# Optimization experiments

Measured on AMD Instinct MI355X. Metric: run time of the kernel, lower is better.

Reference implementation:

```python
import jax, jax.numpy as jnp
import numpy as np
from jax import lax

T, B = 256, 64
VOCAB, D_EMBED, D_HIDDEN = 32000, 512, 1024


def setup_inputs() -> dict:
    key = jax.random.key(0)
    k1, k2, k3, k4 = jax.random.split(key, 4)
    x_seq = jax.random.randint(k1, (T, B), 0, VOCAB, dtype=jnp.int64) if jax.config.jax_enable_x64 else jax.random.randint(k1, (T, B), 0, VOCAB, dtype=jnp.int32)
    scale_e = 1.0
    scale_ih = 1.0 / np.sqrt(D_HIDDEN)
    return {
        "x_seq": x_seq,
        "embedding": jax.random.normal(k2, (VOCAB, D_EMBED), dtype=jnp.float32) * scale_e,
        "W_ih": jax.random.normal(k3, (4 * D_HIDDEN, D_EMBED), dtype=jnp.float32) * scale_ih,
        "W_hh": jax.random.normal(k4, (4 * D_HIDDEN, D_HIDDEN), dtype=jnp.float32) * scale_ih,
        "b_ih": jnp.zeros((4 * D_HIDDEN,), dtype=jnp.float32),
        "b_hh": jnp.zeros((4 * D_HIDDEN,), dtype=jnp.float32),
    }


def reference(x_seq, embedding, W_ih, W_hh, b_ih, b_hh):
    # e_seq: [T, B, E]
    e_seq = embedding[x_seq]
    B_ = x_seq.shape[1]
    H = W_hh.shape[1]
    # Precompute input projections for all timesteps in one big GEMM: [T, B, 4H]
    x_gates = jnp.einsum("tbe,ge->tbg", e_seq, W_ih) + b_ih + b_hh

    def step(carry, xg):
        h, c = carry
        gates = xg + h @ W_hh.T  # [B, 4H]
        i, f, g, o = jnp.split(gates, 4, axis=-1)  # PyTorch gate order i,f,g,o
        i = jax.nn.sigmoid(i)
        f = jax.nn.sigmoid(f)
        g = jnp.tanh(g)
        o = jax.nn.sigmoid(o)
        c_new = f * c + i * g
        h_new = o * jnp.tanh(c_new)
        return (h_new, c_new), h_new

    h0 = jnp.zeros((B_, H), dtype=e_seq.dtype)
    c0 = jnp.zeros((B_, H), dtype=e_seq.dtype)
    (h, c), outs = lax.scan(step, (h0, c0), x_gates)
    return outs, h, c
```

## Files before the change

### kernel.cpp

```cpp
#include <hip/hip_runtime.h>
#include <hip/hip_bf16.h>
#include <cstdint>
#include <cstddef>

#define T_STEPS 256
#define BATCH   64
#define DE      512
#define DH      1024
#define G4      4096
#define NBLK    128

typedef short  bf16x8 __attribute__((ext_vector_type(8)));
typedef float  f32x4  __attribute__((ext_vector_type(4)));
typedef unsigned long long u64;

__device__ __forceinline__ unsigned short bf_bits(__hip_bfloat16 h) {
    union { __hip_bfloat16 h; unsigned short u; } x; x.h = h; return x.u;
}
__device__ __forceinline__ float b2f(unsigned short u) {
    union { float f; unsigned v; } x; x.v = ((unsigned)u) << 16; return x.f;
}

__device__ __forceinline__ void async_copy16(const void* gsrc, void* ldst) {
    __builtin_amdgcn_global_load_lds(
        (const __attribute__((address_space(1))) unsigned int*)gsrc,
        (__attribute__((address_space(3))) unsigned int*)ldst,
        16, 0, 0);
}

__device__ __forceinline__ u64 llc_load64(const u64* p) {
    return __hip_atomic_load(p, __ATOMIC_RELAXED, __HIP_MEMORY_SCOPE_AGENT);
}
__device__ __forceinline__ void llc_store64(u64* p, u64 v) {
    __hip_atomic_store(p, v, __ATOMIC_RELAXED, __HIP_MEMORY_SCOPE_AGENT);
}
__device__ __forceinline__ unsigned llc_load32(const unsigned* p) {
    return __hip_atomic_load(p, __ATOMIC_RELAXED, __HIP_MEMORY_SCOPE_AGENT);
}
__device__ __forceinline__ void llc_store32(unsigned* p, unsigned v) {
    __hip_atomic_store(p, v, __ATOMIC_RELAXED, __HIP_MEMORY_SCOPE_AGENT);
}

__global__ void k_f32_to_bf16(const float* __restrict__ src,
                              __hip_bfloat16* __restrict__ dst, int n8) {
    int i = blockIdx.x * blockDim.x + threadIdx.x;
    if (i >= n8) return;
    const float4* s = (const float4*)src + (size_t)i * 2;
    float4 a = s[0], b = s[1];
    union { unsigned short u[8]; uint4 v; } o;
    o.u[0] = bf_bits(__float2bfloat16(a.x));
    o.u[1] = bf_bits(__float2bfloat16(a.y));
    o.u[2] = bf_bits(__float2bfloat16(a.z));
    o.u[3] = bf_bits(__float2bfloat16(a.w));
    o.u[4] = bf_bits(__float2bfloat16(b.x));
    o.u[5] = bf_bits(__float2bfloat16(b.y));
    o.u[6] = bf_bits(__float2bfloat16(b.z));
    o.u[7] = bf_bits(__float2bfloat16(b.w));
    *((uint4*)dst + i) = o.v;
}

__global__ void k_gather(const int* __restrict__ xs, const float* __restrict__ emb,
                         __hip_bfloat16* __restrict__ e_bf) {
    int tid = blockIdx.x * 256 + threadIdx.x;
    int r = tid >> 6, ch = tid & 63;
    int v = xs[r];
    const float4* s = (const float4*)(emb + (size_t)v * DE + ch * 8);
    float4 a = s[0], b = s[1];
    union { unsigned short u[8]; uint4 v4; } o;
    o.u[0] = bf_bits(__float2bfloat16(a.x));
    o.u[1] = bf_bits(__float2bfloat16(a.y));
    o.u[2] = bf_bits(__float2bfloat16(a.z));
    o.u[3] = bf_bits(__float2bfloat16(a.w));
    o.u[4] = bf_bits(__float2bfloat16(b.x));
    o.u[5] = bf_bits(__float2bfloat16(b.y));
    o.u[6] = bf_bits(__float2bfloat16(b.z));
    o.u[7] = bf_bits(__float2bfloat16(b.w));
    *((uint4*)(e_bf + (size_t)r * DE) + ch) = o.v4;
}

__global__ void k_gemm_xg(const __hip_bfloat16* __restrict__ A,
                          const __hip_bfloat16* __restrict__ Bt,
                          const float* __restrict__ bih, const float* __restrict__ bhh,
                          __hip_bfloat16* __restrict__ xgp) {
    __shared__ __align__(16) __hip_bfloat16 sA[128 * 32];
    __shared__ __align__(16) __hip_bfloat16 sB[128 * 32];
    const int bm = blockIdx.x >> 5;
    const int bn = blockIdx.x & 31;
    const int tid = threadIdx.x;
    const int l = tid & 63, w = tid >> 6;
    const int wm = w >> 1, wn = w & 1;
    const int lrow = l & 15, lq = l >> 4;

    f32x4 acc[4][4] = {};

    for (int kb = 0; kb < 512; kb += 32) {
#pragma unroll
        for (int q = 0; q < 2; ++q) {
            int c = q * 256 + tid;
            int row = c >> 2, seg = c & 3;
            async_copy16(A + (size_t)(bm * 128 + row) * 512 + kb + seg * 8, &sA[c * 8]);
            async_copy16(Bt + (size_t)(bn * 128 + row) * 512 + kb + seg * 8, &sB[c * 8]);
        }
        __syncthreads();
        bf16x8 af[4], bq[4];
#pragma unroll
        for (int mt = 0; mt < 4; ++mt)
            af[mt] = *(const bf16x8*)&sA[(wm * 64 + mt * 16 + lrow) * 32 + lq * 8];
#pragma unroll
        for (int nt = 0; nt < 4; ++nt)
            bq[nt] = *(const bf16x8*)&sB[(wn * 64 + nt * 16 + lrow) * 32 + lq * 8];
#pragma unroll
        for (int mt = 0; mt < 4; ++mt)
#pragma unroll
            for (int nt = 0; nt < 4; ++nt)
                acc[mt][nt] = __builtin_amdgcn_mfma_f32_16x16x32_bf16(
                    af[mt], bq[nt], acc[mt][nt], 0, 0, 0);
        __syncthreads();
    }

#pragma unroll
    for (int nt = 0; nt < 4; ++nt) {
        int n = bn * 128 + wn * 64 + nt * 16 + lrow;
        int g = n >> 10, j = n & 1023, blk = j >> 3, u = j & 7;
        float bias = bih[n] + bhh[n];
#pragma unroll
        for (int mt = 0; mt < 4; ++mt) {
#pragma unroll
            for (int r = 0; r < 4; ++r) {
                int m = bm * 128 + wm * 64 + mt * 16 + lq * 4 + r;
                int t = m >> 6, b = m & 63;
                xgp[(((size_t)(t * NBLK + blk) * 4 + g) * 8 + u) * 64 + b] =
                    __float2bfloat16(acc[mt][nt][r] + bias);
            }
        }
    }
}

__global__ void __launch_bounds__(256) k_lstm(
        const __hip_bfloat16* __restrict__ xgp,
        const __hip_bfloat16* __restrict__ Whh,
        __hip_bfloat16* __restrict__ hbuf,
        float* __restrict__ out,
        unsigned* __restrict__ flags) {
    __shared__ __hip_bfloat16 sW[32768];
    __shared__ __align__(8) __hip_bfloat16 sPack[512];
    const int tid = threadIdx.x, l = tid & 63, w = tid >> 6;
    const int lrow = l & 15, lq = l >> 4;
    const int bk = blockIdx.x;

#pragma unroll
    for (int f = 0; f < 16; ++f) {
        int fi = f * 256 + tid;
        int col = fi & 15, q = (fi >> 4) & 3, kb = (fi >> 6) & 31, nt = fi >> 11;
        int g = (nt * 16 + col) >> 3, u = col & 7;
        async_copy16(Whh + (size_t)(g * DH + bk * 8 + u) * DH + kb * 32 + q * 8,
                     &sW[fi * 8]);
    }
    if (tid < 128)
        llc_store64((u64*)hbuf + bk * 128 + tid, 0ull);
    asm volatile("s_waitcnt vmcnt(0)" ::: "memory");
    __syncthreads();
    if (tid == 0) llc_store32(&flags[bk], 1u);
    if (tid < 128)
        while (llc_load32(&flags[tid]) < 1u) __builtin_amdgcn_s_sleep(2);
    __syncthreads();

    const int u = l & 7, halfsel = (l >> 3) & 1;
    const int b0 = w * 16 + lq * 4;
    const int aib = lq * 128 + w * 32 + lrow * 2;
    float creg[4] = {0.f, 0.f, 0.f, 0.f};

    for (int t = 0; t < T_STEPS; ++t) {
        const u64* hin  = (const u64*)hbuf + (size_t)(t % 3) * 16384;
        u64*       hout = (u64*)hbuf + (size_t)((t + 1) % 3) * 16384;

        const __hip_bfloat16* xgt = xgp + (size_t)t * (NBLK * 2048) + (size_t)bk * 2048;
        ushort4 x0 = *(const ushort4*)(xgt + (halfsel * 8 + u) * 64 + b0);
        ushort4 x1 = *(const ushort4*)(xgt + ((2 + halfsel) * 8 + u) * 64 + b0);

        u64 alo[8], ahi[8];
#pragma unroll
        for (int p = 0; p < 8; ++p) {
            alo[p] = llc_load64(hin + p * 512 + aib);
            ahi[p] = llc_load64(hin + p * 512 + aib + 1);
        }
        f32x4 a00 = {}, a01 = {}, a10 = {}, a11 = {};
#pragma unroll
        for (int kb = 0; kb < 32; ++kb) {
            union { u64 q[2]; bf16x8 v; } A;
            A.q[0] = alo[kb & 7]; A.q[1] = ahi[kb & 7];
            bf16x8 b0f = *(const bf16x8*)&sW[(kb * 4 + lq) * 128 + lrow * 8];
            bf16x8 b1f = *(const bf16x8*)&sW[16384 + (kb * 4 + lq) * 128 + lrow * 8];
            if (kb & 1) {
                a01 = __builtin_amdgcn_mfma_f32_16x16x32_bf16(A.v, b0f, a01, 0, 0, 0);
                a11 = __builtin_amdgcn_mfma_f32_16x16x32_bf16(A.v, b1f, a11, 0, 0, 0);
            } else {
                a00 = __builtin_amdgcn_mfma_f32_16x16x32_bf16(A.v, b0f, a00, 0, 0, 0);
                a10 = __builtin_amdgcn_mfma_f32_16x16x32_bf16(A.v, b1f, a10, 0, 0, 0);
            }
            if (kb + 8 < 32) {
                alo[kb & 7] = llc_load64(hin + (kb + 8) * 512 + aib);
                ahi[kb & 7] = llc_load64(hin + (kb + 8) * 512 + aib + 1);
            }
        }
        f32x4 A0 = a00 + a01, A1 = a10 + a11;

        const unsigned short xs0[4] = {x0.x, x0.y, x0.z, x0.w};
        const unsigned short xs1[4] = {x1.x, x1.y, x1.z, x1.w};
#pragma unroll
        for (int r = 0; r < 4; ++r) {
            float v0 = A0[r] + b2f(xs0[r]);
            float v1 = A1[r] + b2f(xs1[r]);
            float p0 = __shfl_xor(v0, 8, 64);
            float p1 = __shfl_xor(v1, 8, 64);
            float ipre = halfsel ? p0 : v0;
            float fpre = halfsel ? v0 : p0;
            float gpre = halfsel ? p1 : v1;
            float opre = halfsel ? v1 : p1;
            if (!halfsel) {
                float ig = 1.0f / (1.0f + __expf(-ipre));
                float fg = 1.0f / (1.0f + __expf(-fpre));
                float gg = tanhf(gpre);
                float og = 1.0f / (1.0f + __expf(-opre));
                float cnew = fg * creg[r] + ig * gg;
                float hnew = og * tanhf(cnew);
                creg[r] = cnew;
                int b = b0 + r;
                int j = bk * 8 + u;
                sPack[b * 8 + u] = __float2bfloat16(hnew);
                out[(size_t)t * (BATCH * DH) + b * DH + j] = hnew;
                if (t == T_STEPS - 1) {
                    out[(size_t)T_STEPS * BATCH * DH + b * DH + j] = hnew;
                    out[(size_t)T_STEPS * BATCH * DH + BATCH * DH + b * DH + j] = cnew;
                }
            }
        }
        __syncthreads();
        if (tid < 128)
            llc_store64(hout + bk * 128 + tid, *(const u64*)&sPack[tid * 4]);
        if (t < T_STEPS - 1) {
            asm volatile("s_waitcnt vmcnt(0)" ::: "memory");
            __syncthreads();
            if (tid == 0) llc_store32(&flags[bk], (unsigned)(t + 2));
            if (tid < 128)
                while (llc_load32(&flags[tid]) < (unsigned)(t + 2))
                    __builtin_amdgcn_s_sleep(2);
            __syncthreads();
        }
    }
}

extern "C" void kernel_launch(void* const* d_in, const int* in_sizes, int n_in,
                              void* d_out, int out_size, void* d_ws, size_t ws_size,
                              hipStream_t stream) {
    const int*   xs  = (const int*)d_in[0];
    const float* emb = (const float*)d_in[1];
    const float* Wih = (const float*)d_in[2];
    const float* Whh = (const float*)d_in[3];
    const float* bih = (const float*)d_in[4];
    const float* bhh = (const float*)d_in[5];
    float* out = (float*)d_out;
    char*  ws  = (char*)d_ws;

    __hip_bfloat16* Wih_bf = (__hip_bfloat16*)(ws);
    __hip_bfloat16* Whh_bf = (__hip_bfloat16*)(ws + 4194304);
    __hip_bfloat16* e_bf   = (__hip_bfloat16*)(ws + 12582912);
    __hip_bfloat16* xgp    = (__hip_bfloat16*)(ws + 29360128);
    __hip_bfloat16* hbuf   = (__hip_bfloat16*)(ws + 163577856);
    unsigned*       flags  = (unsigned*)(ws + 163971072);

    hipMemsetAsync(flags, 0, 512, stream);
    k_f32_to_bf16<<<1024, 256, 0, stream>>>(Wih, Wih_bf, 2097152 / 8);
    k_f32_to_bf16<<<2048, 256, 0, stream>>>(Whh, Whh_bf, 4194304 / 8);
    k_gather<<<4096, 256, 0, stream>>>(xs, emb, e_bf);
    k_gemm_xg<<<4096, 256, 0, stream>>>(e_bf, Wih_bf, bih, bhh, xgp);
    k_lstm<<<NBLK, 256, 0, stream>>>(xgp, Whh_bf, hbuf, out, flags);
}
```

Before: 2.236 ms.

## Restructure LSTM step sync, h layout, and output stores off the critical path

The per-step flag wait is now done by every wave, each reading the flags as 64-bit pairs, which replaces the 128-thread spin and trailing block barrier. The output h store moves after the flag publish so it overlaps the wait. The h exchange buffer is re-laid out so each lane reads its 32 A-fragments contiguously, all issued up front instead of through a rolling 8-deep prefetch. launch_bounds adds a minimum of one block per SM. The cost is higher register pressure from holding 64 u64 loads and more flag polling traffic from all waves.

```diff
diff --git a/kernel.cpp b/kernel.cpp
--- a/kernel.cpp
+++ b/kernel.cpp
@@ -136,7 +136,7 @@
     }
 }
 
-__global__ void __launch_bounds__(256) k_lstm(
+__global__ void __launch_bounds__(256, 1) k_lstm(
         const __hip_bfloat16* __restrict__ xgp,
         const __hip_bfloat16* __restrict__ Whh,
         __hip_bfloat16* __restrict__ hbuf,
@@ -168,6 +168,10 @@
     const int u = l & 7, halfsel = (l >> 3) & 1;
     const int b0 = w * 16 + lq * 4;
     const int aib = lq * 128 + w * 32 + lrow * 2;
+    const int jout = bk * 8 + u;
+    const u64* f64 = (const u64*)flags;
+    const int pst_c = ((bk & 3) << 7) + tid;
+    const int pst_idx = ((pst_c >> 1) << 6) + ((bk >> 2) << 1) + (pst_c & 1);
     float creg[4] = {0.f, 0.f, 0.f, 0.f};
 
     for (int t = 0; t < T_STEPS; ++t) {
@@ -178,17 +182,19 @@
         ushort4 x0 = *(const ushort4*)(xgt + (halfsel * 8 + u) * 64 + b0);
         ushort4 x1 = *(const ushort4*)(xgt + ((2 + halfsel) * 8 + u) * 64 + b0);
 
-        u64 alo[8], ahi[8];
-#pragma unroll
-        for (int p = 0; p < 8; ++p) {
-            alo[p] = llc_load64(hin + p * 512 + aib);
-            ahi[p] = llc_load64(hin + p * 512 + aib + 1);
-        }
+        const u64* hl = hin + ((aib >> 1) << 6);
+        u64 alo[32], ahi[32];
+#pragma unroll
+        for (int p = 0; p < 32; ++p) {
+            alo[p] = llc_load64(hl + 2 * p);
+            ahi[p] = llc_load64(hl + 2 * p + 1);
+        }
+
         f32x4 a00 = {}, a01 = {}, a10 = {}, a11 = {};
 #pragma unroll
         for (int kb = 0; kb < 32; ++kb) {
             union { u64 q[2]; bf16x8 v; } A;
-            A.q[0] = alo[kb & 7]; A.q[1] = ahi[kb & 7];
+            A.q[0] = alo[kb]; A.q[1] = ahi[kb];
             bf16x8 b0f = *(const bf16x8*)&sW[(kb * 4 + lq) * 128 + lrow * 8];
             bf16x8 b1f = *(const bf16x8*)&sW[16384 + (kb * 4 + lq) * 128 + lrow * 8];
             if (kb & 1) {
@@ -198,15 +204,12 @@
                 a00 = __builtin_amdgcn_mfma_f32_16x16x32_bf16(A.v, b0f, a00, 0, 0, 0);
                 a10 = __builtin_amdgcn_mfma_f32_16x16x32_bf16(A.v, b1f, a10, 0, 0, 0);
             }
-            if (kb + 8 < 32) {
-                alo[kb & 7] = llc_load64(hin + (kb + 8) * 512 + aib);
-                ahi[kb & 7] = llc_load64(hin + (kb + 8) * 512 + aib + 1);
-            }
         }
         f32x4 A0 = a00 + a01, A1 = a10 + a11;
 
         const unsigned short xs0[4] = {x0.x, x0.y, x0.z, x0.w};
         const unsigned short xs1[4] = {x1.x, x1.y, x1.z, x1.w};
+        float hreg[4] = {0.f, 0.f, 0.f, 0.f};
 #pragma unroll
         for (int r = 0; r < 4; ++r) {
             float v0 = A0[r] + b2f(xs0[r]);
@@ -225,27 +228,40 @@
                 float cnew = fg * creg[r] + ig * gg;
                 float hnew = og * tanhf(cnew);
                 creg[r] = cnew;
-                int b = b0 + r;
-                int j = bk * 8 + u;
-                sPack[b * 8 + u] = __float2bfloat16(hnew);
-                out[(size_t)t * (BATCH * DH) + b * DH + j] = hnew;
-                if (t == T_STEPS - 1) {
-                    out[(size_t)T_STEPS * BATCH * DH + b * DH + j] = hnew;
-                    out[(size_t)T_STEPS * BATCH * DH + BATCH * DH + b * DH + j] = cnew;
+                hreg[r] = hnew;
+                sPack[(b0 + r) * 8 + u] = __float2bfloat16(hnew);
+            }
+        }
+
+        if (t == T_STEPS - 1) {
+            if (!halfsel) {
+#pragma unroll
+                for (int r = 0; r < 4; ++r) {
+                    int b = b0 + r;
+                    out[(size_t)t * (BATCH * DH) + b * DH + jout] = hreg[r];
+                    out[(size_t)T_STEPS * BATCH * DH + b * DH + jout] = hreg[r];
+                    out[(size_t)T_STEPS * BATCH * DH + BATCH * DH + b * DH + jout] = creg[r];
                 }
             }
-        }
-        __syncthreads();
-        if (tid < 128)
-            llc_store64(hout + bk * 128 + tid, *(const u64*)&sPack[tid * 4]);
-        if (t < T_STEPS - 1) {
+        } else {
+            __syncthreads();
+            if (tid < 128)
+                llc_store64(hout + pst_idx, *(const u64*)&sPack[tid * 4]);
             asm volatile("s_waitcnt vmcnt(0)" ::: "memory");
             __syncthreads();
             if (tid == 0) llc_store32(&flags[bk], (unsigned)(t + 2));
-            if (tid < 128)
-                while (llc_load32(&flags[tid]) < (unsigned)(t + 2))
-                    __builtin_amdgcn_s_sleep(2);
-            __syncthreads();
+            if (!halfsel) {
+#pragma unroll
+                for (int r = 0; r < 4; ++r)
+                    out[(size_t)t * (BATCH * DH) + (b0 + r) * DH + jout] = hreg[r];
+            }
+            const unsigned need = (unsigned)(t + 2);
+            while (true) {
+                u64 fv = llc_load64(f64 + l);
+                if ((unsigned)fv >= need && (unsigned)(fv >> 32) >= need) break;
+                __builtin_amdgcn_s_sleep(2);
+            }
+            asm volatile("" ::: "memory");
         }
     }
 }
```

New measurement: 4.303 ms. 92.5% more time.
